# Kernel optimization log

Hardware: AMD Instinct MI355X
Metric: run time of the kernel (lower is better)

Reference implementation:

```python
import jax, jax.numpy as jnp
import numpy as np

STRIDE = (1, 1)
PAD = (1, 1)
DIL = (1, 1)
KH, KW = 3, 3
DEFORM_GROUPS = 2


def setup_inputs() -> dict:
    key = jax.random.key(0)
    ks = jax.random.split(key, 5)
    B, C, H, W = 4, 128, 64, 64
    Cout = 128
    K = KH * KW
    n = C * KH * KW
    stdv = 1.0 / np.sqrt(n)
    x = jax.random.normal(ks[0], (B, C, H, W), dtype=jnp.float32)
    offset = jax.random.normal(ks[1], (B, DEFORM_GROUPS * 2 * K, H, W), dtype=jnp.float32)
    mask = jax.random.uniform(ks[2], (B, DEFORM_GROUPS * K, H, W), dtype=jnp.float32)
    weight = jax.random.uniform(ks[3], (Cout, C, KH, KW), minval=-stdv, maxval=stdv, dtype=jnp.float32)
    bias = jnp.zeros((Cout,), dtype=jnp.float32)
    return {"x": x, "offset": offset, "mask": mask, "weight": weight, "bias": bias}


def _mdcn_forward(x, offset, mask, weight, bias):
    B, C, H, W = x.shape
    Cout, Cin_g, kh, kw = weight.shape
    K = kh * kw
    dg = offset.shape[1] // (2 * K)
    Cg = C // dg
    sh, sw = STRIDE
    ph, pw = PAD
    dh, dw = DIL
    Ho = (H + 2 * ph - (dh * (kh - 1) + 1)) // sh + 1
    Wo = (W + 2 * pw - (dw * (kw - 1) + 1)) // sw + 1

    # offsets: (B, dg, K, 2, Ho, Wo) with (dy, dx) pairs; mask: (B, dg, K, Ho, Wo)
    off = offset.reshape(B, dg, K, 2, Ho, Wo)
    m = mask.reshape(B, dg, K, Ho, Wo)

    ky, kx = jnp.meshgrid(jnp.arange(kh), jnp.arange(kw), indexing="ij")
    ky = ky.reshape(K).astype(x.dtype)  # kernel tap row offsets
    kx = kx.reshape(K).astype(x.dtype)
    oy = (jnp.arange(Ho) * sh - ph).astype(x.dtype)
    ox = (jnp.arange(Wo) * sw - pw).astype(x.dtype)

    # sampling positions (B, dg, K, Ho, Wo)
    py = off[:, :, :, 0] + oy[None, None, None, :, None] + (ky * dh)[None, None, :, None, None]
    px = off[:, :, :, 1] + ox[None, None, None, None, :] + (kx * dw)[None, None, :, None, None]

    y0 = jnp.floor(py)
    x0 = jnp.floor(px)
    ly = py - y0
    lx = px - x0
    y0i = y0.astype(jnp.int32)
    x0i = x0.astype(jnp.int32)

    xg = x.reshape(B, dg, Cg, H * W)

    def gather(yi, xi):
        valid = (yi >= 0) & (yi < H) & (xi >= 0) & (xi < W)
        idx = jnp.clip(yi, 0, H - 1) * W + jnp.clip(xi, 0, W - 1)  # (B,dg,K,Ho,Wo)
        g = jax.vmap(jax.vmap(lambda xf, ix: xf[:, ix]))(xg, idx.reshape(B, dg, K * Ho * Wo))
        g = g.reshape(B, dg, Cg, K, Ho, Wo)
        return g * valid[:, :, None].astype(x.dtype)

    w00 = ((1 - ly) * (1 - lx))[:, :, None]
    w01 = ((1 - ly) * lx)[:, :, None]
    w10 = (ly * (1 - lx))[:, :, None]
    w11 = (ly * lx)[:, :, None]

    val = (w00 * gather(y0i, x0i)
           + w01 * gather(y0i, x0i + 1)
           + w10 * gather(y0i + 1, x0i)
           + w11 * gather(y0i + 1, x0i + 1))

    # modulation and im2col-GEMM (groups=1): col (B, C*K, Ho*Wo)
    col = (val * m[:, :, None]).reshape(B, C * K, Ho * Wo)
    wk = weight.reshape(Cout, C * K)
    out = jnp.einsum("ok,bkp->bop", wk, col).reshape(B, Cout, Ho, Wo)
    return out + bias[None, :, None, None]


def reference(x, offset, mask, weight, bias):
    return _mdcn_forward(x, offset, mask, weight, bias)
```

## Files before the change

### kernel.cpp

```cpp
#include <hip/hip_runtime.h>
#include <hip/hip_fp16.h>

#define B_    4
#define C_    128
#define H_    64
#define W_    64
#define CO_   128
#define K_    9
#define DG_   2
#define HW_   4096
#define CK_   1152
#define NKT_  36
#define NPAIR_ 576
#define PSTR_ 68
#define PLSZ_ 4352
#define LSTR_ 580

typedef __attribute__((ext_vector_type(8))) short  short8;
typedef __attribute__((ext_vector_type(4))) float  floatx4;
typedef float f2v __attribute__((ext_vector_type(2), aligned(4)));

__device__ __align__(16) unsigned short g_wA[NKT_ * 8 * 64 * 8];
__device__ __align__(16) unsigned int   g_colu[(size_t)B_ * 256 * NPAIR_ * 16];
__device__ __align__(16) int4           g_desc[B_ * DG_ * K_ * HW_];

__device__ __forceinline__ unsigned short f32_to_bf16(float f) {
    unsigned int u = __float_as_uint(f);
    u += 0x7FFFu + ((u >> 16) & 1u);
    return (unsigned short)(u >> 16);
}
__device__ __forceinline__ unsigned int pack_bf16x2(float a, float b) {
    return (unsigned int)f32_to_bf16(a) | ((unsigned int)f32_to_bf16(b) << 16);
}

__global__ __launch_bounds__(256) void prep_kernel(
    const float* __restrict__ w,
    const float* __restrict__ offset,
    const float* __restrict__ mask)
{
    const int bid = blockIdx.x;
    if (bid < 576) {
        const int lin  = bid * 256 + threadIdx.x;
        const int j    = lin & 7;
        const int lane = (lin >> 3) & 63;
        const int mtkt = lin >> 9;
        const int mt   = mtkt & 7;
        const int kt   = mtkt >> 3;
        const int co   = mt * 16 + (lane & 15);
        const int k    = kt * 32 + (lane >> 4) * 8 + j;
        g_wA[lin] = f32_to_bf16(w[co * CK_ + k]);
    } else {
        const int lin = (bid - 576) * 256 + threadIdx.x;
        const int pix = lin & (HW_ - 1);
        const int bgk = lin >> 12;
        const int k   = bgk % 9;
        const int bg  = bgk / 9;
        const int ho = pix >> 6;
        const int wo = pix & 63;
        const int ky = k / 3;
        const int kx = k - 3 * ky;

        const float py = offset[(size_t)(bg * 18 + 2 * k)     * HW_ + pix] + (float)(ho - 1 + ky);
        const float px = offset[(size_t)(bg * 18 + 2 * k + 1) * HW_ + pix] + (float)(wo - 1 + kx);
        const float m  = mask  [(size_t)(bg * 9 + k)          * HW_ + pix];

        const float y0f = floorf(py);
        const float x0f = floorf(px);
        const float ly = py - y0f;
        const float lx = px - x0f;
        const int y0 = (int)y0f;
        const int x0 = (int)x0f;

        const bool yin = (y0 >= 0) & (y0 <= H_ - 2);
        const float er0 = yin ? (1.0f - ly) : ((y0 == -1)     ? ly          : 0.0f);
        const float er1 = yin ? ly          : ((y0 == H_ - 1) ? (1.0f - ly) : 0.0f);
        const bool xin = (x0 >= 0) & (x0 <= W_ - 2);
        const float ec0 = xin ? (1.0f - lx) : ((x0 == -1)     ? lx          : 0.0f);
        const float ec1 = xin ? lx          : ((x0 == W_ - 1) ? (1.0f - lx) : 0.0f);
        const int yc = min(max(y0, 0), H_ - 2);
        const int xc = min(max(x0, 0), W_ - 2);

        const __half2 wlo = __floats2half2_rn(m * er0 * ec0, m * er0 * ec1);
        const __half2 whi = __floats2half2_rn(m * er1 * ec0, m * er1 * ec1);
        int4 d;
        d.x = yc * PSTR_ + xc;
        d.y = __builtin_bit_cast(int, wlo);
        d.z = __builtin_bit_cast(int, whi);
        d.w = 0;
        g_desc[lin] = d;
    }
}

__global__ __launch_bounds__(1024, 4) void col_kernel(const float* __restrict__ x)
{
    const int bid = blockIdx.x;
    const int b   = bid >> 6;
    const int cp  = bid & 63;
    const int c0  = cp * 2;
    const int g   = c0 >> 6;
    const int t   = threadIdx.x;

    __shared__ __align__(16) float s_x[2 * PLSZ_];

    {
        const int ci = t >> 9;
        const int q  = t & 511;
        const float* __restrict__ src = x + (size_t)(b * C_ + c0 + ci) * HW_ + q * 8;
        const float4 v0 = *(const float4*)src;
        const float4 v1 = *(const float4*)(src + 4);
        float* dst = s_x + ci * PLSZ_ + (q >> 3) * PSTR_ + (q & 7) * 8;
        *(float4*)dst = v0;
        *(float4*)(dst + 4) = v1;
    }
    __syncthreads();

    const int4* __restrict__ descb = g_desc + (size_t)((b * DG_ + g) * 9) * HW_;

#pragma unroll
    for (int ps = 0; ps < 4; ++ps) {
        const int pix = ps * 1024 + t;
        const int pt  = pix >> 4;
        const int pl  = pix & 15;
        int4 d[9];
#pragma unroll
        for (int k = 0; k < 9; ++k) d[k] = descb[(size_t)k * HW_ + pix];

        float v[18];
#pragma unroll
        for (int k = 0; k < 9; ++k) {
            const float2 wl = __half22float2(__builtin_bit_cast(__half2, d[k].y));
            const float2 wh = __half22float2(__builtin_bit_cast(__half2, d[k].z));
#pragma unroll
            for (int ci = 0; ci < 2; ++ci) {
                const float* p = s_x + ci * PLSZ_ + d[k].x;
                const f2v lo = *(const f2v*)p;
                const f2v hi = *(const f2v*)(p + PSTR_);
                v[ci * 9 + k] = wl.x * lo.x + wl.y * lo.y + wh.x * hi.x + wh.y * hi.y;
            }
        }
        unsigned int* __restrict__ outb =
            g_colu + ((size_t)(b * 256 + pt) * NPAIR_ + cp * 9) * 16 + pl;
#pragma unroll
        for (int j = 0; j < 9; ++j)
            outb[j * 16] = pack_bf16x2(v[2 * j], v[2 * j + 1]);
    }
}

__global__ __launch_bounds__(256, 4) void gemm_kernel(
    const float* __restrict__ bias, float* __restrict__ out)
{
    const int bid  = blockIdx.x;
    const int b    = bid >> 8;
    const int pt   = bid & 255;
    const int t    = threadIdx.x;

    __shared__ __align__(16) unsigned int s_b[16 * LSTR_];

    {
        const uint4* __restrict__ src =
            (const uint4*)(g_colu + (size_t)(b * 256 + pt) * (NPAIR_ * 16));
#pragma unroll
        for (int i = 0; i < 9; ++i) {
            const int c = i * 256 + t;
            const uint4 v = src[c];
            const int pair = c >> 2;
            const int plc  = (c & 3) * 4;
            s_b[(plc + 0) * LSTR_ + pair] = v.x;
            s_b[(plc + 1) * LSTR_ + pair] = v.y;
            s_b[(plc + 2) * LSTR_ + pair] = v.z;
            s_b[(plc + 3) * LSTR_ + pair] = v.w;
        }
    }
    __syncthreads();

    const int wv   = t >> 6;
    const int lane = t & 63;
    const int l15  = lane & 15;
    const int quad = lane >> 4;

    const unsigned short* __restrict__ ap =
        g_wA + ((size_t)(wv * 2) * 64 + lane) * 8;
    const unsigned int* bp = s_b + l15 * LSTR_ + quad * 4;

    floatx4 acc0 = {0.f, 0.f, 0.f, 0.f};
    floatx4 acc1 = {0.f, 0.f, 0.f, 0.f};

    short8 a0c = *(const short8*)ap;
    short8 a1c = *(const short8*)(ap + 512);
    short8 b_c = __builtin_bit_cast(short8, *(const uint4*)bp);

#pragma unroll 4
    for (int kt = 0; kt < NKT_; ++kt) {
        short8 a0n = a0c, a1n = a1c, b_n = b_c;
        if (kt < NKT_ - 1) {
            const unsigned short* an = ap + (size_t)(kt + 1) * 4096;
            a0n = *(const short8*)an;
            a1n = *(const short8*)(an + 512);
            b_n = __builtin_bit_cast(short8, *(const uint4*)(bp + (kt + 1) * 16));
        }
        acc0 = __builtin_amdgcn_mfma_f32_16x16x32_bf16(a0c, b_c, acc0, 0, 0, 0);
        acc1 = __builtin_amdgcn_mfma_f32_16x16x32_bf16(a1c, b_c, acc1, 0, 0, 0);
        a0c = a0n; a1c = a1n; b_c = b_n;
    }

#pragma unroll
    for (int mt = 0; mt < 2; ++mt) {
        const floatx4 a = mt ? acc1 : acc0;
        const int cob = wv * 32 + mt * 16 + quad * 4;
#pragma unroll
        for (int r = 0; r < 4; ++r) {
            const int co = cob + r;
            out[((size_t)(b * CO_ + co) << 12) + pt * 16 + l15] = a[r] + bias[co];
        }
    }
}

extern "C" void kernel_launch(void* const* d_in, const int* in_sizes, int n_in,
                              void* d_out, int out_size, void* d_ws, size_t ws_size,
                              hipStream_t stream) {
    const float* x      = (const float*)d_in[0];
    const float* offset = (const float*)d_in[1];
    const float* mask   = (const float*)d_in[2];
    const float* weight = (const float*)d_in[3];
    const float* bias   = (const float*)d_in[4];
    float* out = (float*)d_out;

    hipLaunchKernelGGL(prep_kernel, dim3(576 + 1152), dim3(256), 0, stream, weight, offset, mask);
    hipLaunchKernelGGL(col_kernel, dim3(B_ * 64), dim3(1024), 0, stream, x);
    hipLaunchKernelGGL(gemm_kernel, dim3(B_ * 256), dim3(256), 0, stream, bias, out);
}
```

Before: 107.0 us.

## Widen GEMM pixel tile to 32 and read B operand directly from global

The col buffer layout changes to 32-pixel tiles, and the GEMM kernel now uses 512-thread blocks with 8 waves split over Cout and two 16-pixel halves. The LDS staging and transpose of the B operand is dropped: each lane loads four scalar dwords straight from global memory per k-step. This removes the LDS fill, the barrier and the shared memory footprint. In exchange, B loads become strided 4-byte global accesses that rely on L1/L2, and each B element is fetched by four waves.

```diff
diff --git a/kernel.cpp b/kernel.cpp
--- a/kernel.cpp
+++ b/kernel.cpp
@@ -14,14 +14,13 @@
 #define NPAIR_ 576
 #define PSTR_ 68
 #define PLSZ_ 4352
-#define LSTR_ 580
 
 typedef __attribute__((ext_vector_type(8))) short  short8;
 typedef __attribute__((ext_vector_type(4))) float  floatx4;
 typedef float f2v __attribute__((ext_vector_type(2), aligned(4)));
 
 __device__ __align__(16) unsigned short g_wA[NKT_ * 8 * 64 * 8];
-__device__ __align__(16) unsigned int   g_colu[(size_t)B_ * 256 * NPAIR_ * 16];
+__device__ __align__(16) unsigned int   g_colu[(size_t)B_ * 128 * NPAIR_ * 32];
 __device__ __align__(16) int4           g_desc[B_ * DG_ * K_ * HW_];
 
 __device__ __forceinline__ unsigned short f32_to_bf16(float f) {
@@ -119,8 +118,8 @@
 #pragma unroll
     for (int ps = 0; ps < 4; ++ps) {
         const int pix = ps * 1024 + t;
-        const int pt  = pix >> 4;
-        const int pl  = pix & 15;
+        const int pt  = pix >> 5;
+        const int pl  = pix & 31;
         int4 d[9];
 #pragma unroll
         for (int k = 0; k < 9; ++k) d[k] = descb[(size_t)k * HW_ + pix];
@@ -139,55 +138,39 @@
             }
         }
         unsigned int* __restrict__ outb =
-            g_colu + ((size_t)(b * 256 + pt) * NPAIR_ + cp * 9) * 16 + pl;
+            g_colu + ((size_t)(b * 128 + pt) * NPAIR_ + cp * 9) * 32 + pl;
 #pragma unroll
         for (int j = 0; j < 9; ++j)
-            outb[j * 16] = pack_bf16x2(v[2 * j], v[2 * j + 1]);
-    }
-}
-
-__global__ __launch_bounds__(256, 4) void gemm_kernel(
+            outb[j * 32] = pack_bf16x2(v[2 * j], v[2 * j + 1]);
+    }
+}
+
+__global__ __launch_bounds__(512) void gemm_kernel(
     const float* __restrict__ bias, float* __restrict__ out)
 {
     const int bid  = blockIdx.x;
-    const int b    = bid >> 8;
-    const int pt   = bid & 255;
+    const int b    = bid >> 7;
+    const int pt   = bid & 127;
     const int t    = threadIdx.x;
-
-    __shared__ __align__(16) unsigned int s_b[16 * LSTR_];
-
-    {
-        const uint4* __restrict__ src =
-            (const uint4*)(g_colu + (size_t)(b * 256 + pt) * (NPAIR_ * 16));
-#pragma unroll
-        for (int i = 0; i < 9; ++i) {
-            const int c = i * 256 + t;
-            const uint4 v = src[c];
-            const int pair = c >> 2;
-            const int plc  = (c & 3) * 4;
-            s_b[(plc + 0) * LSTR_ + pair] = v.x;
-            s_b[(plc + 1) * LSTR_ + pair] = v.y;
-            s_b[(plc + 2) * LSTR_ + pair] = v.z;
-            s_b[(plc + 3) * LSTR_ + pair] = v.w;
-        }
-    }
-    __syncthreads();
-
-    const int wv   = t >> 6;
+    const int w    = t >> 6;
+    const int cw   = w >> 1;
+    const int nt   = w & 1;
     const int lane = t & 63;
     const int l15  = lane & 15;
     const int quad = lane >> 4;
 
-    const unsigned short* __restrict__ ap =
-        g_wA + ((size_t)(wv * 2) * 64 + lane) * 8;
-    const unsigned int* bp = s_b + l15 * LSTR_ + quad * 4;
+    const unsigned short* __restrict__ ap = g_wA + ((size_t)(cw * 2) * 64 + lane) * 8;
+    const unsigned int* __restrict__ bp =
+        g_colu + ((size_t)(b * 128 + pt) * NPAIR_ + quad * 4) * 32 + nt * 16 + l15;
 
     floatx4 acc0 = {0.f, 0.f, 0.f, 0.f};
     floatx4 acc1 = {0.f, 0.f, 0.f, 0.f};
 
     short8 a0c = *(const short8*)ap;
     short8 a1c = *(const short8*)(ap + 512);
-    short8 b_c = __builtin_bit_cast(short8, *(const uint4*)bp);
+    uint4 u0;
+    u0.x = bp[0]; u0.y = bp[32]; u0.z = bp[64]; u0.w = bp[96];
+    short8 b_c = __builtin_bit_cast(short8, u0);
 
 #pragma unroll 4
     for (int kt = 0; kt < NKT_; ++kt) {
@@ -196,7 +179,10 @@
             const unsigned short* an = ap + (size_t)(kt + 1) * 4096;
             a0n = *(const short8*)an;
             a1n = *(const short8*)(an + 512);
-            b_n = __builtin_bit_cast(short8, *(const uint4*)(bp + (kt + 1) * 16));
+            const unsigned int* bq = bp + (size_t)(kt + 1) * 512;
+            uint4 u;
+            u.x = bq[0]; u.y = bq[32]; u.z = bq[64]; u.w = bq[96];
+            b_n = __builtin_bit_cast(short8, u);
         }
         acc0 = __builtin_amdgcn_mfma_f32_16x16x32_bf16(a0c, b_c, acc0, 0, 0, 0);
         acc1 = __builtin_amdgcn_mfma_f32_16x16x32_bf16(a1c, b_c, acc1, 0, 0, 0);
@@ -204,13 +190,13 @@
     }
 
 #pragma unroll
-    for (int mt = 0; mt < 2; ++mt) {
-        const floatx4 a = mt ? acc1 : acc0;
-        const int cob = wv * 32 + mt * 16 + quad * 4;
+    for (int mtl = 0; mtl < 2; ++mtl) {
+        const floatx4 a = mtl ? acc1 : acc0;
+        const int cob = cw * 32 + mtl * 16 + quad * 4;
 #pragma unroll
         for (int r = 0; r < 4; ++r) {
             const int co = cob + r;
-            out[((size_t)(b * CO_ + co) << 12) + pt * 16 + l15] = a[r] + bias[co];
+            out[((size_t)(b * CO_ + co) << 12) + pt * 32 + nt * 16 + l15] = a[r] + bias[co];
         }
     }
 }
@@ -227,5 +213,5 @@
 
     hipLaunchKernelGGL(prep_kernel, dim3(576 + 1152), dim3(256), 0, stream, weight, offset, mask);
     hipLaunchKernelGGL(col_kernel, dim3(B_ * 64), dim3(1024), 0, stream, x);
-    hipLaunchKernelGGL(gemm_kernel, dim3(B_ * 256), dim3(256), 0, stream, bias, out);
-}
+    hipLaunchKernelGGL(gemm_kernel, dim3(B_ * 128), dim3(512), 0, stream, bias, out);
+}
```

After: 102.6 us. 1.04x faster.
